# Performance work log

Measured on AMD Instinct MI355X. Metric: run time of the kernel, lower is better.

Reference implementation:

```python
import jax, jax.numpy as jnp
import numpy as np

GRID_SIZE = 5
GRID_LO, GRID_HI = -1.0, 1.0


def setup_inputs() -> dict:
    key = jax.random.key(0)
    k1, k2 = jax.random.split(key)
    B, out_dim, in_dim, H, W = 8, 64, 64, 192, 192
    G = GRID_SIZE + 1
    x = jax.random.normal(k1, (B, in_dim, H, W), dtype=jnp.float32)
    coef = jax.random.normal(k2, (B, out_dim, in_dim, G), dtype=jnp.float32) * 0.1
    return {"x": x, "coef": coef}


def reference(x, coef):
    # x: [B, in_dim, H, W]; coef: [B, out_dim, in_dim, G] with G = grid_size + 1
    G = GRID_SIZE + 1
    grid = jnp.linspace(GRID_LO, GRID_HI, G, dtype=x.dtype)
    lo, hi = grid[0], grid[-1]
    spacing = grid[1] - grid[0]

    B, in_dim, H, W = x.shape
    out_dim = coef.shape[1]
    P = H * W

    xf = x.reshape(B, in_dim, P)
    xc = jnp.clip(xf, lo, hi)
    nx = (xc - lo) / spacing                      # normalized coordinate in [0, grid_size]
    idx = jnp.clip(jnp.floor(nx).astype(jnp.int32), 0, GRID_SIZE - 1)  # left knot
    frac = nx - idx.astype(x.dtype)               # fractional offset (grad flows via nx)
    w1 = 1.0 - frac
    w2 = frac
    idx_next = jnp.clip(idx + 1, 0, GRID_SIZE)    # right knot (max index = G-1)

    # Two-hot interpolation weights over the G grid points: [B, in, P, G]
    Wt = (w1[..., None] * jax.nn.one_hot(idx, G, dtype=x.dtype)
          + w2[..., None] * jax.nn.one_hot(idx_next, G, dtype=x.dtype))

    # result[b,o,p] = sum_i sum_g Wt[b,i,p,g] * coef[b,o,i,g]
    out = jnp.einsum('bipg,boig->bop', Wt, coef)
    return out.reshape(B, out_dim, H, W)
```

## Files before the change

kernel.cpp:

```cpp
#include <hip/hip_runtime.h>
#include <stdint.h>


typedef __fp16 half8_t __attribute__((ext_vector_type(8)));
typedef __fp16 half2_t __attribute__((ext_vector_type(2)));
typedef float f32x4 __attribute__((ext_vector_type(4)));

#define NBATCH 8
#define OD 64
#define ID 64
#define PIX 36864
#define NG 6
#define PT 192
#define KI 16
#define NCHUNK 4
#define AROW 104
#define XROW 18
#define PTILES (PIX / PT)

__global__ __launch_bounds__(256, 2)
void kan_mfma(const float* __restrict__ x, const float* __restrict__ coef,
              float* __restrict__ out) {
  const int t = threadIdx.x;
  const int lane = t & 63;
  const int wave = t >> 6;
  const int q8 = lane >> 4;
  const int col = lane & 15;

  const int bid = blockIdx.x;
  const int b = bid / PTILES;
  const int ptile = bid % PTILES;
  const int p0 = ptile * PT;

  __shared__ __fp16 A_lds[OD][AROW] __attribute__((aligned(16)));
  __shared__ float nx_lds[PT][XROW] __attribute__((aligned(16)));

  f32x4 acc[4][3];
#pragma unroll
  for (int i = 0; i < 4; ++i)
#pragma unroll
    for (int j = 0; j < 3; ++j)
      acc[i][j] = (f32x4){0.f, 0.f, 0.f, 0.f};

  const float* xb = x + (size_t)b * ID * PIX + p0;
  const float* cb = coef + (size_t)b * OD * ID * NG;

  const int iof0 = (q8 & 1) * 8;
  const int ghalf = q8 >> 1;

  for (int c = 0; c < NCHUNK; ++c) {
    const int i0 = c * KI;
    __syncthreads();

#pragma unroll
    for (int j = 0; j < (KI * PT) / 256; ++j) {
      int lin = j * 256 + t;
      int p = lin % PT;
      int iof = lin / PT;
      float xv = xb[(size_t)(i0 + iof) * PIX + p];
      xv = fminf(fmaxf(xv, -1.f), 1.f);
      nx_lds[p][iof] = (xv + 1.f) * 2.5f;
    }

    {
      const int o = t >> 2;
      const int r0 = (t & 3) * 24;
      const float* crow = cb + o * (ID * NG) + i0 * NG + r0;
#pragma unroll
      for (int j = 0; j < 24; ++j) {
        int r = r0 + j;
        int iof = r / 6;
        int g = r - iof * 6;
        A_lds[o][g * KI + iof] = (__fp16)crow[j];
      }
    }
    __syncthreads();

    float nxv[3][8];
#pragma unroll
    for (int pti = 0; pti < 3; ++pti) {
      int p = wave * 48 + pti * 16 + col;
#pragma unroll
      for (int j = 0; j < 8; ++j)
        nxv[pti][j] = nx_lds[p][iof0 + j];
    }

#pragma unroll
    for (int ks = 0; ks < 3; ++ks) {
      half8_t af[4];
#pragma unroll
      for (int ot = 0; ot < 4; ++ot)
        af[ot] = *(const half8_t*)&A_lds[ot * 16 + col][ks * 32 + q8 * 8];

      const float gf = (float)(2 * ks + ghalf);
#pragma unroll
      for (int pti = 0; pti < 3; ++pti) {
        union { half2_t h2[4]; half8_t v; } bu;
#pragma unroll
        for (int jj = 0; jj < 4; ++jj) {
          float h0 = fmaxf(0.f, 1.f - fabsf(nxv[pti][2 * jj] - gf));
          float h1 = fmaxf(0.f, 1.f - fabsf(nxv[pti][2 * jj + 1] - gf));
          bu.h2[jj] = __builtin_amdgcn_cvt_pkrtz(h0, h1);
        }
#pragma unroll
        for (int ot = 0; ot < 4; ++ot)
          acc[ot][pti] = __builtin_amdgcn_mfma_f32_16x16x32_f16(
              af[ot], bu.v, acc[ot][pti], 0, 0, 0);
      }
    }
  }

  float* ob = out + (size_t)b * OD * PIX + p0;
#pragma unroll
  for (int ot = 0; ot < 4; ++ot) {
#pragma unroll
    for (int pti = 0; pti < 3; ++pti) {
      int p = wave * 48 + pti * 16 + col;
#pragma unroll
      for (int r = 0; r < 4; ++r) {
        int o = ot * 16 + q8 * 4 + r;
        ob[(size_t)o * PIX + p] = acc[ot][pti][r];
      }
    }
  }
}

extern "C" void kernel_launch(void* const* d_in, const int* in_sizes, int n_in,
                              void* d_out, int out_size, void* d_ws, size_t ws_size,
                              hipStream_t stream) {
  const float* x = (const float*)d_in[0];
  const float* coef = (const float*)d_in[1];
  float* out = (float*)d_out;
  dim3 grid(NBATCH * PTILES);
  dim3 block(256);
  hipLaunchKernelGGL(kan_mfma, grid, block, 0, stream, x, coef, out);
}
```

Measured before the change: 151.4 us.

## Precompute fp16 coef layout in workspace and stream A fragments from global

Adds a prep kernel that converts coef to fp16 in the MFMA fragment order and stores it in the workspace. The main kernel now reads A fragments straight from global (L2-cached) instead of staging them through LDS each chunk. It also doubles K per chunk to 32 input channels, loads x with vectorized float4 reads and prefetches the next chunk into registers, and transposes the nx LDS layout. The goal is to cut per-block coef conversion, LDS traffic and barriers, at the cost of an extra launch and global reads for A. A fallback kernel keeps the old path when the workspace is too small.

```diff
diff --git a/kernel.cpp b/kernel.cpp
--- a/kernel.cpp
+++ b/kernel.cpp
@@ -12,15 +12,32 @@
 #define PIX 36864
 #define NG 6
 #define PT 192
-#define KI 16
-#define NCHUNK 4
-#define AROW 104
-#define XROW 18
+#define KI 32
+#define NCHUNK 2
+#define KROW 384
+#define PROW 196
 #define PTILES (PIX / PT)
 
-__global__ __launch_bounds__(256, 2)
-void kan_mfma(const float* __restrict__ x, const float* __restrict__ coef,
-              float* __restrict__ out) {
+#define CPRE_BYTES (NBATCH * OD * KROW * 2)
+
+__global__ __launch_bounds__(256)
+void prep_coef(const float* __restrict__ coef, __fp16* __restrict__ cpre) {
+  int idx = blockIdx.x * 256 + threadIdx.x;
+  int b = idx / (OD * KROW);
+  int rem = idx % (OD * KROW);
+  int o = rem / KROW;
+  int k = rem % KROW;
+  int c = k / 192;
+  int s = k % 192;
+  int g = s >> 5;
+  int iof = s & 31;
+  float v = coef[((size_t)(b * OD + o) * ID + c * KI + iof) * NG + g];
+  cpre[idx] = (__fp16)v;
+}
+
+__global__ __launch_bounds__(256, 3)
+void kan_mfma2(const float* __restrict__ x, const __fp16* __restrict__ cpre,
+               float* __restrict__ out) {
   const int t = threadIdx.x;
   const int lane = t & 63;
   const int wave = t >> 6;
@@ -29,11 +46,9 @@
 
   const int bid = blockIdx.x;
   const int b = bid / PTILES;
-  const int ptile = bid % PTILES;
-  const int p0 = ptile * PT;
-
-  __shared__ __fp16 A_lds[OD][AROW] __attribute__((aligned(16)));
-  __shared__ float nx_lds[PT][XROW] __attribute__((aligned(16)));
+  const int p0 = (bid % PTILES) * PT;
+
+  __shared__ float nx_lds[KI][PROW] __attribute__((aligned(16)));
 
   f32x4 acc[4][3];
 #pragma unroll
@@ -43,38 +58,36 @@
       acc[i][j] = (f32x4){0.f, 0.f, 0.f, 0.f};
 
   const float* xb = x + (size_t)b * ID * PIX + p0;
-  const float* cb = coef + (size_t)b * OD * ID * NG;
-
-  const int iof0 = (q8 & 1) * 8;
-  const int ghalf = q8 >> 1;
-
+  const __fp16* caw = cpre + (size_t)b * OD * KROW + (size_t)col * KROW + q8 * 8;
+  const int srow = t >> 3;
+  const int pb = (t & 7) * 24;
+
+  f32x4 xv[6];
+#pragma unroll
+  for (int j = 0; j < 6; ++j)
+    xv[j] = *(const f32x4*)(xb + (size_t)srow * PIX + pb + 4 * j);
+
+#pragma unroll
   for (int c = 0; c < NCHUNK; ++c) {
-    const int i0 = c * KI;
+    if (c > 0) __syncthreads();
+
+#pragma unroll
+    for (int j = 0; j < 6; ++j) {
+      f32x4 n;
+#pragma unroll
+      for (int r = 0; r < 4; ++r) {
+        float v = fminf(fmaxf(xv[j][r], -1.f), 1.f);
+        n[r] = (v + 1.f) * 2.5f;
+      }
+      *(f32x4*)&nx_lds[srow][pb + 4 * j] = n;
+    }
     __syncthreads();
 
-#pragma unroll
-    for (int j = 0; j < (KI * PT) / 256; ++j) {
-      int lin = j * 256 + t;
-      int p = lin % PT;
-      int iof = lin / PT;
-      float xv = xb[(size_t)(i0 + iof) * PIX + p];
-      xv = fminf(fmaxf(xv, -1.f), 1.f);
-      nx_lds[p][iof] = (xv + 1.f) * 2.5f;
-    }
-
-    {
-      const int o = t >> 2;
-      const int r0 = (t & 3) * 24;
-      const float* crow = cb + o * (ID * NG) + i0 * NG + r0;
-#pragma unroll
-      for (int j = 0; j < 24; ++j) {
-        int r = r0 + j;
-        int iof = r / 6;
-        int g = r - iof * 6;
-        A_lds[o][g * KI + iof] = (__fp16)crow[j];
-      }
-    }
-    __syncthreads();
+    if (c + 1 < NCHUNK) {
+#pragma unroll
+      for (int j = 0; j < 6; ++j)
+        xv[j] = *(const f32x4*)(xb + (size_t)(KI + srow) * PIX + pb + 4 * j);
+    }
 
     float nxv[3][8];
 #pragma unroll
@@ -82,17 +95,18 @@
       int p = wave * 48 + pti * 16 + col;
 #pragma unroll
       for (int j = 0; j < 8; ++j)
-        nxv[pti][j] = nx_lds[p][iof0 + j];
-    }
-
-#pragma unroll
-    for (int ks = 0; ks < 3; ++ks) {
+        nxv[pti][j] = nx_lds[q8 * 8 + j][p];
+    }
+
+    const __fp16* cac = caw + c * 192;
+#pragma unroll
+    for (int ks = 0; ks < 6; ++ks) {
       half8_t af[4];
 #pragma unroll
       for (int ot = 0; ot < 4; ++ot)
-        af[ot] = *(const half8_t*)&A_lds[ot * 16 + col][ks * 32 + q8 * 8];
-
-      const float gf = (float)(2 * ks + ghalf);
+        af[ot] = *(const half8_t*)(cac + (size_t)(ot * 16) * KROW + ks * 32);
+
+      const float gf = (float)ks;
 #pragma unroll
       for (int pti = 0; pti < 3; ++pti) {
         union { half2_t h2[4]; half8_t v; } bu;
@@ -123,6 +137,102 @@
       }
     }
   }
+}
+
+#define AROW 104
+#define XROW 18
+__global__ __launch_bounds__(256, 2)
+void kan_mfma_fb(const float* __restrict__ x, const float* __restrict__ coef,
+                 float* __restrict__ out) {
+  const int t = threadIdx.x;
+  const int lane = t & 63;
+  const int wave = t >> 6;
+  const int q8 = lane >> 4;
+  const int col = lane & 15;
+  const int bid = blockIdx.x;
+  const int b = bid / PTILES;
+  const int p0 = (bid % PTILES) * PT;
+
+  __shared__ __fp16 A_lds[OD][AROW] __attribute__((aligned(16)));
+  __shared__ float nxf[PT][XROW] __attribute__((aligned(16)));
+
+  f32x4 acc[4][3];
+#pragma unroll
+  for (int i = 0; i < 4; ++i)
+#pragma unroll
+    for (int j = 0; j < 3; ++j) acc[i][j] = (f32x4){0.f, 0.f, 0.f, 0.f};
+
+  const float* xb = x + (size_t)b * ID * PIX + p0;
+  const float* cb = coef + (size_t)b * OD * ID * NG;
+  const int iof0 = (q8 & 1) * 8;
+  const int ghalf = q8 >> 1;
+
+  for (int c = 0; c < 4; ++c) {
+    const int i0 = c * 16;
+    __syncthreads();
+#pragma unroll
+    for (int j = 0; j < 12; ++j) {
+      int lin = j * 256 + t;
+      int p = lin % PT;
+      int iof = lin / PT;
+      float xvv = xb[(size_t)(i0 + iof) * PIX + p];
+      xvv = fminf(fmaxf(xvv, -1.f), 1.f);
+      nxf[p][iof] = (xvv + 1.f) * 2.5f;
+    }
+    {
+      const int o = t >> 2;
+      const int r0 = (t & 3) * 24;
+      const float* crow = cb + o * (ID * NG) + i0 * NG + r0;
+#pragma unroll
+      for (int j = 0; j < 24; ++j) {
+        int r = r0 + j;
+        int iof = r / 6;
+        int g = r - iof * 6;
+        A_lds[o][g * 16 + iof] = (__fp16)crow[j];
+      }
+    }
+    __syncthreads();
+
+    float nxv[3][8];
+#pragma unroll
+    for (int pti = 0; pti < 3; ++pti) {
+      int p = wave * 48 + pti * 16 + col;
+#pragma unroll
+      for (int j = 0; j < 8; ++j) nxv[pti][j] = nxf[p][iof0 + j];
+    }
+#pragma unroll
+    for (int ks = 0; ks < 3; ++ks) {
+      half8_t af[4];
+#pragma unroll
+      for (int ot = 0; ot < 4; ++ot)
+        af[ot] = *(const half8_t*)&A_lds[ot * 16 + col][ks * 32 + q8 * 8];
+      const float gf = (float)(2 * ks + ghalf);
+#pragma unroll
+      for (int pti = 0; pti < 3; ++pti) {
+        union { half2_t h2[4]; half8_t v; } bu;
+#pragma unroll
+        for (int jj = 0; jj < 4; ++jj) {
+          float h0 = fmaxf(0.f, 1.f - fabsf(nxv[pti][2 * jj] - gf));
+          float h1 = fmaxf(0.f, 1.f - fabsf(nxv[pti][2 * jj + 1] - gf));
+          bu.h2[jj] = __builtin_amdgcn_cvt_pkrtz(h0, h1);
+        }
+#pragma unroll
+        for (int ot = 0; ot < 4; ++ot)
+          acc[ot][pti] = __builtin_amdgcn_mfma_f32_16x16x32_f16(
+              af[ot], bu.v, acc[ot][pti], 0, 0, 0);
+      }
+    }
+  }
+  float* ob = out + (size_t)b * OD * PIX + p0;
+#pragma unroll
+  for (int ot = 0; ot < 4; ++ot)
+#pragma unroll
+    for (int pti = 0; pti < 3; ++pti) {
+      int p = wave * 48 + pti * 16 + col;
+#pragma unroll
+      for (int r = 0; r < 4; ++r)
+        ob[(size_t)(ot * 16 + q8 * 4 + r) * PIX + p] = acc[ot][pti][r];
+    }
 }
 
 extern "C" void kernel_launch(void* const* d_in, const int* in_sizes, int n_in,
@@ -131,7 +241,14 @@
   const float* x = (const float*)d_in[0];
   const float* coef = (const float*)d_in[1];
   float* out = (float*)d_out;
-  dim3 grid(NBATCH * PTILES);
-  dim3 block(256);
-  hipLaunchKernelGGL(kan_mfma, grid, block, 0, stream, x, coef, out);
-}
+  if (ws_size >= (size_t)CPRE_BYTES) {
+    __fp16* cpre = (__fp16*)d_ws;
+    hipLaunchKernelGGL(prep_coef, dim3((NBATCH * OD * KROW) / 256), dim3(256), 0,
+                       stream, coef, cpre);
+    hipLaunchKernelGGL(kan_mfma2, dim3(NBATCH * PTILES), dim3(256), 0, stream, x,
+                       cpre, out);
+  } else {
+    hipLaunchKernelGGL(kan_mfma_fb, dim3(NBATCH * PTILES), dim3(256), 0, stream,
+                       x, coef, out);
+  }
+}
```

New measurement: 159.7 us. 1.05x slower.
